# Kernel optimization log

Measured on AMD Instinct MI355X. Metric: run time of the kernel, lower is better.

Reference implementation:

```python
import jax, jax.numpy as jnp
import numpy as np
import math

NQ = 8            # n_qubits (hardcoded in _TransformerBlockQuantum)
DIM = 2 ** NQ     # statevector size = 256
H = 16            # num_heads
EPS = 1e-5        # LayerNorm eps

# PauliZ expectation table: wire 0 = most significant bit. ZTAB[w, j] = +/-1
_bits = (np.arange(DIM)[None, :] >> (NQ - 1 - np.arange(NQ)[:, None])) & 1
ZTAB = (1.0 - 2.0 * _bits).astype(np.float32)  # [NQ, DIM]


def _apply_1q(state, gate, w):
    # state: [N, 2^NQ] complex, gate: [N, 2, 2] complex, acts on wire w (MSB ordering)
    N = state.shape[0]
    s = state.reshape(N, 2 ** w, 2, 2 ** (NQ - w - 1))
    s = jnp.einsum('nab,npbq->npaq', gate, s)
    return s.reshape(N, DIM)


def _apply_cnot(state, c):
    # CNOT with control wire c, target wire c+1 (adjacent chain)
    N = state.shape[0]
    s = state.reshape(N, 2 ** c, 2, 2, 2 ** (NQ - c - 2))
    s = jnp.concatenate([s[:, :, :1], jnp.flip(s[:, :, 1:], axis=3)], axis=2)
    return s.reshape(N, DIM)


def _layernorm(x, g, b):
    mu = jnp.mean(x, axis=-1, keepdims=True)
    var = jnp.mean((x - mu) ** 2, axis=-1, keepdims=True)
    return (x - mu) / jnp.sqrt(var + EPS) * g + b


def _quantum_ffn(x, Win, b_in, Wout, b_out, ry):
    B, S, D = x.shape
    ang = (jnp.einsum('bsd,qd->bsq', x, Win) + b_in).reshape(-1, NQ)  # [N, NQ]
    N = ang.shape[0]
    state = jnp.zeros((N, DIM), jnp.complex64).at[:, 0].set(1.0)
    # RX encoding (per-token angles)
    for w in range(NQ):
        th = ang[:, w] * 0.5
        c, s = jnp.cos(th), jnp.sin(th)
        g = jnp.stack([jnp.stack([c, -1j * s], -1), jnp.stack([-1j * s, c], -1)], -2)
        state = _apply_1q(state, g.astype(jnp.complex64), w)
    # trainable RY (shared angles)
    for w in range(NQ):
        th = ry[w] * 0.5
        c, s = jnp.cos(th), jnp.sin(th)
        g = jnp.stack([jnp.stack([c, -s]), jnp.stack([s, c])]).astype(jnp.complex64)
        state = _apply_1q(state, jnp.broadcast_to(g, (N, 2, 2)), w)
    # CNOT entangling chain
    for w in range(NQ - 1):
        state = _apply_cnot(state, w)
    probs = jnp.abs(state) ** 2                      # [N, DIM] float32
    expz = probs @ ZTAB.T                            # [N, NQ]
    out = jnp.einsum('bsq,dq->bsd', expz.reshape(B, S, NQ), Wout) + b_out
    return jax.nn.relu(out)  # dropout = identity in eval


def _forward(x, Wq, Wk, Wv, Wo, g1, b1, g2, b2, Win, b_in, Wout, b_out, ry):
    B, S, D = x.shape
    dk = D // H
    q = jnp.einsum('bsd,ed->bse', x, Wq).reshape(B, S, H, dk)
    k = jnp.einsum('bsd,ed->bse', x, Wk).reshape(B, S, H, dk)
    v = jnp.einsum('bsd,ed->bse', x, Wv).reshape(B, S, H, dk)
    scores = jnp.einsum('bqhd,bkhd->bhqk', q, k) / math.sqrt(dk)
    attn = jax.nn.softmax(scores, axis=-1)
    o = jnp.einsum('bhqk,bkhd->bqhd', attn, v).reshape(B, S, D)
    attn_out = jnp.einsum('bsd,ed->bse', o, Wo)
    x1 = _layernorm(x + attn_out, g1, b1)
    ffn_out = _quantum_ffn(x1, Win, b_in, Wout, b_out, ry)
    return _layernorm(x1 + ffn_out, g2, b2)


def setup_inputs() -> dict:
    key = jax.random.key(0)
    ks = jax.random.split(key, 16)
    B, S, D = 2, 2048, 1024
    sd = 1.0 / math.sqrt(D)
    return {
        'x': jax.random.normal(ks[0], (B, S, D), jnp.float32),
        'Wq': jax.random.normal(ks[1], (D, D), jnp.float32) * sd,
        'Wk': jax.random.normal(ks[2], (D, D), jnp.float32) * sd,
        'Wv': jax.random.normal(ks[3], (D, D), jnp.float32) * sd,
        'Wo': jax.random.normal(ks[4], (D, D), jnp.float32) * sd,
        'g1': jnp.ones((D,), jnp.float32),
        'b1': jnp.zeros((D,), jnp.float32),
        'g2': jnp.ones((D,), jnp.float32),
        'b2': jnp.zeros((D,), jnp.float32),
        'Win': jax.random.normal(ks[5], (NQ, D), jnp.float32) * sd,
        'b_in': jnp.zeros((NQ,), jnp.float32),
        'Wout': jax.random.normal(ks[6], (D, NQ), jnp.float32) * (1.0 / math.sqrt(NQ)),
        'b_out': jnp.zeros((D,), jnp.float32),
        'ry': jax.random.normal(ks[7], (NQ,), jnp.float32) * 0.1,
    }


def reference(x, Wq, Wk, Wv, Wo, g1, b1, g2, b2, Win, b_in, Wout, b_out, ry):
    return _forward(x, Wq, Wk, Wv, Wo, g1, b1, g2, b2, Win, b_in, Wout, b_out, ry)
```

## Files before the change

kernel.cpp:

```cpp
#include <hip/hip_runtime.h>
#include <stdint.h>


typedef unsigned short u16;
typedef unsigned int   u32;
typedef __bf16 bf16x8 __attribute__((ext_vector_type(8)));
typedef u16    u16x8  __attribute__((ext_vector_type(8)));
typedef u16    u16x4  __attribute__((ext_vector_type(4)));
typedef float  f32x4  __attribute__((ext_vector_type(4)));

#define DEV static __device__ __forceinline__

DEV u16 f2b(float f){ u32 u = __float_as_uint(f); return (u16)((u + 0x7fffu + ((u>>16)&1u)) >> 16); }

#define MFMA16(a,b,c) __builtin_amdgcn_mfma_f32_16x16x32_bf16((a),(b),(c),0,0,0)
#define GLD16(gp,lp) __builtin_amdgcn_global_load_lds( \
    (const __attribute__((address_space(1))) u32*)(const void*)(gp), \
    (__attribute__((address_space(3))) u32*)(void*)(lp), 16, 0, 0)

__global__ __launch_bounds__(256) void k_cast(const float* __restrict__ src, u16* __restrict__ dst){
  const int i = blockIdx.x*256 + threadIdx.x;
  const f32x4* s = (const f32x4*)src + (size_t)i*2;
  f32x4 a = s[0], b = s[1];
  u16x8 o;
  o[0]=f2b(a.x); o[1]=f2b(a.y); o[2]=f2b(a.z); o[3]=f2b(a.w);
  o[4]=f2b(b.x); o[5]=f2b(b.y); o[6]=f2b(b.z); o[7]=f2b(b.w);
  ((u16x8*)dst)[i] = o;
}

__global__ __launch_bounds__(256) void k_cast_w(
    const float* __restrict__ Wq, const float* __restrict__ Wk,
    const float* __restrict__ Wv, const float* __restrict__ Wo,
    u16* __restrict__ wb, u16* __restrict__ wob){
  const int r = blockIdx.x >> 9, bi = blockIdx.x & 511;
  const float* src = (r==0)?Wq:((r==1)?Wk:((r==2)?Wv:Wo));
  u16* dst = (r<3) ? (wb + (size_t)r*1048576) : wob;
  const int i = bi*256 + threadIdx.x;
  const f32x4* s = (const f32x4*)src + (size_t)i*2;
  f32x4 a = s[0], b = s[1];
  u16x8 o;
  o[0]=f2b(a.x); o[1]=f2b(a.y); o[2]=f2b(a.z); o[3]=f2b(a.w);
  o[4]=f2b(b.x); o[5]=f2b(b.y); o[6]=f2b(b.z); o[7]=f2b(b.w);
  ((u16x8*)dst)[i] = o;
}

template<int MODE>
__global__ __launch_bounds__(256) void k_gemm_nt(
    const u16* __restrict__ A, const u16* __restrict__ B,
    float* __restrict__ Cf, u16* __restrict__ Qo, u16* __restrict__ Ko, u16* __restrict__ Vt,
    int K, int N)
{
  __shared__ __attribute__((aligned(16))) u16 As[128*64];
  __shared__ __attribute__((aligned(16))) u16 Bs[128*64];
  const int tid = threadIdx.x, lane = tid & 63, w = tid >> 6;
  const int wr = w >> 1, wc = w & 1;
  const int m0 = blockIdx.y*128, n0 = blockIdx.x*128;
  const int l15 = lane & 15, lg = lane >> 4;
  f32x4 acc[4][4] = {};
  const int lr = lane >> 3, lc = (lane & 7)*8;
  const u16* ag = A + (size_t)(m0 + w*32 + lr)*K + lc;
  const u16* bg = B + (size_t)(n0 + w*32 + lr)*K + lc;
  u16* asl = &As[(w*32)*64];
  u16* bsl = &Bs[(w*32)*64];
  for (int k0 = 0; k0 < K; k0 += 64){
    __syncthreads();
    #pragma unroll
    for (int c = 0; c < 4; ++c){
      GLD16(ag + (size_t)(c*8)*K + k0, asl + c*512);
      GLD16(bg + (size_t)(c*8)*K + k0, bsl + c*512);
    }
    __syncthreads();
    #pragma unroll
    for (int kk = 0; kk < 2; ++kk){
      const int ko = kk*32 + lg*8;
      bf16x8 af[4], bf[4];
      #pragma unroll
      for (int t=0;t<4;++t) af[t] = *(const bf16x8*)&As[(wr*64 + t*16 + l15)*64 + ko];
      #pragma unroll
      for (int t=0;t<4;++t) bf[t] = *(const bf16x8*)&Bs[(wc*64 + t*16 + l15)*64 + ko];
      #pragma unroll
      for (int i=0;i<4;++i)
        #pragma unroll
        for (int j=0;j<4;++j)
          acc[i][j] = MFMA16(af[i], bf[j], acc[i][j]);
    }
  }
  const int col0 = n0 + wc*64 + l15;
  const int row0 = m0 + wr*64 + lg*4;
  if (MODE==0){
    const int which = n0 >> 10;
    if (which == 2){
      #pragma unroll
      for (int i=0;i<4;++i){
        const int rr0 = row0 + i*16;
        const int bsel = rr0 >> 11, ss = rr0 & 2047;
        #pragma unroll
        for (int j=0;j<4;++j){
          const int d_loc = (col0 + j*16) & 1023;
          const int hh = d_loc >> 6, dd = d_loc & 63;
          u16x4 pk;
          #pragma unroll
          for (int r=0;r<4;++r) pk[r] = f2b(acc[i][j][r]);
          *(u16x4*)(Vt + ((size_t)((bsel*16 + hh)*64 + dd))*2048 + ss) = pk;
        }
      }
    } else {
      u16* dst = which ? Ko : Qo;
      const float scl = which ? 1.f : 0.125f;
      #pragma unroll
      for (int i=0;i<4;++i)
      #pragma unroll
      for (int j=0;j<4;++j){
        const int cc = (col0 + j*16) & 1023;
        #pragma unroll
        for (int r=0;r<4;++r)
          dst[(size_t)(row0 + i*16 + r)*1024 + cc] = f2b(acc[i][j][r]*scl);
      }
    }
  } else {
    #pragma unroll
    for (int i=0;i<4;++i)
    #pragma unroll
    for (int j=0;j<4;++j){
      const int cc = col0 + j*16;
      #pragma unroll
      for (int r=0;r<4;++r)
        Cf[(size_t)(row0 + i*16 + r)*N + cc] = acc[i][j][r];
    }
  }
}

__global__ __launch_bounds__(256) void k_attn(
    const u16* __restrict__ q, const u16* __restrict__ k,
    const u16* __restrict__ vt, u16* __restrict__ o)
{
  __shared__ __attribute__((aligned(16))) char KVb[2][16384];
  __shared__ __attribute__((aligned(16))) u16 Ps[4][1024];
  const int tid = threadIdx.x, lane = tid & 63, w = tid >> 6;
  const int p = blockIdx.x >> 5, qt = blockIdx.x & 31;
  const int b = p >> 4, h = p & 15;
  const int t0 = b*2048 + qt*64 + w*16;
  const int l15 = lane & 15, lg = lane >> 4;
  const int swz = (l15 & 7) << 4;
  bf16x8 qa[2];
  #pragma unroll
  for (int kk=0;kk<2;++kk)
    qa[kk] = *(const bf16x8*)(q + (size_t)(t0 + l15)*1024 + h*64 + kk*32 + lg*8);
  const char* kgl[2]; const char* vgl[2]; int ldsK[2], ldsV[2];
  #pragma unroll
  for (int i=0;i<2;++i){
    const int s = w*2048 + i*1024 + lane*16;
    const int row = s >> 7;
    const int cb = (s & 127) ^ ((row & 7) << 4);
    kgl[i] = (const char*)k  + ((size_t)(b*2048 + row))*2048 + h*128 + cb;
    vgl[i] = (const char*)vt + ((size_t)(p*64    + row))*4096 + cb;
    ldsK[i] = w*2048 + i*1024;
    ldsV[i] = 8192 + w*2048 + i*1024;
  }
  f32x4 oacc[4] = {};
  float mrow = -1e30f, lrow = 0.f;
  int cur = 0;
  #pragma unroll
  for (int i=0;i<2;++i){ GLD16(kgl[i], KVb[0] + ldsK[i]); GLD16(vgl[i], KVb[0] + ldsV[i]); }
  for (int it = 0; it < 32; ++it){
    __syncthreads();
    if (it < 31){
      const size_t nkv = (size_t)(it+1)*64;
      #pragma unroll
      for (int i=0;i<2;++i){
        GLD16(kgl[i] + nkv*2048, KVb[cur^1] + ldsK[i]);
        GLD16(vgl[i] + nkv*2,    KVb[cur^1] + ldsV[i]);
      }
    }
    const char* Kb = KVb[cur];
    const char* Vb = KVb[cur] + 8192;
    f32x4 sacc[4] = {};
    #pragma unroll
    for (int kk=0;kk<2;++kk){
      const int co = (kk*64 + lg*16) ^ swz;
      bf16x8 kbf[4];
      #pragma unroll
      for (int nt=0;nt<4;++nt) kbf[nt] = *(const bf16x8*)(Kb + (nt*16 + l15)*128 + co);
      #pragma unroll
      for (int nt=0;nt<4;++nt) sacc[nt] = MFMA16(kbf[nt], qa[kk], sacc[nt]);
    }
    float mx = sacc[0][0];
    #pragma unroll
    for (int nt=0;nt<4;++nt)
      #pragma unroll
      for (int r=0;r<4;++r) mx = fmaxf(mx, sacc[nt][r]);
    mx = fmaxf(mx, __shfl_xor(mx, 16));
    mx = fmaxf(mx, __shfl_xor(mx, 32));
    const float mnew = fmaxf(mrow, mx);
    const float scl = __expf(mrow - mnew);
    mrow = mnew;
    float rsum = 0.f;
    #pragma unroll
    for (int nt=0;nt<4;++nt)
      #pragma unroll
      for (int r=0;r<4;++r){ float e = __expf(sacc[nt][r] - mnew); sacc[nt][r] = e; rsum += e; }
    rsum += __shfl_xor(rsum, 16);
    rsum += __shfl_xor(rsum, 32);
    lrow = lrow*scl + rsum;
    char* Pw = (char*)&Ps[w][0];
    #pragma unroll
    for (int nt=0;nt<4;++nt){
      u16x4 pk;
      #pragma unroll
      for (int r=0;r<4;++r) pk[r] = f2b(sacc[nt][r]);
      *(u16x4*)(Pw + l15*128 + (((nt*16 + lg*4)*2) ^ swz)) = pk;
    }
    float sclo[4];
    #pragma unroll
    for (int r=0;r<4;++r) sclo[r] = __shfl(scl, lg*4 + r);
    #pragma unroll
    for (int nt=0;nt<4;++nt)
      #pragma unroll
      for (int r=0;r<4;++r) oacc[nt][r] *= sclo[r];
    #pragma unroll
    for (int kk=0;kk<2;++kk){
      const int co = (kk*64 + lg*16) ^ swz;
      bf16x8 pf = *(const bf16x8*)(Pw + l15*128 + co);
      bf16x8 vf[4];
      #pragma unroll
      for (int nt=0;nt<4;++nt) vf[nt] = *(const bf16x8*)(Vb + (nt*16 + l15)*128 + co);
      #pragma unroll
      for (int nt=0;nt<4;++nt) oacc[nt] = MFMA16(pf, vf[nt], oacc[nt]);
    }
    cur ^= 1;
  }
  float rl[4];
  #pragma unroll
  for (int r=0;r<4;++r){ float lf = __shfl(lrow, lg*4 + r); rl[r] = 1.f/lf; }
  #pragma unroll
  for (int nt=0;nt<4;++nt)
  #pragma unroll
  for (int r=0;r<4;++r)
    o[(size_t)(t0 + lg*4 + r)*1024 + h*64 + nt*16 + l15] = f2b(oacc[nt][r]*rl[r]);
}

__global__ __launch_bounds__(256) void k_tail(
    const float* __restrict__ x, const float* __restrict__ attn,
    const float* __restrict__ g1, const float* __restrict__ b1,
    const float* __restrict__ Win, const float* __restrict__ b_in,
    const float* __restrict__ Wout, const float* __restrict__ b_out,
    const float* __restrict__ ry,
    const float* __restrict__ g2, const float* __restrict__ b2,
    float* __restrict__ out)
{
  const int tid = threadIdx.x, lane = tid & 63, w = tid >> 6;
  const int t = blockIdx.x*4 + w;
  const size_t base = (size_t)t*1024;
  f32x4 yv[4];
  float s1 = 0.f, s2 = 0.f;
  #pragma unroll
  for (int c=0;c<4;++c){
    const int idx = c*256 + lane*4;
    f32x4 xv = *(const f32x4*)(x + base + idx);
    f32x4 av = *(const f32x4*)(attn + base + idx);
    f32x4 y = xv + av;
    yv[c] = y;
    s1 += y.x + y.y + y.z + y.w;
    s2 += y.x*y.x + y.y*y.y + y.z*y.z + y.w*y.w;
  }
  #pragma unroll
  for (int off=32; off; off>>=1){ s1 += __shfl_xor(s1, off); s2 += __shfl_xor(s2, off); }
  {
    const float mu = s1*(1.f/1024.f);
    const float rinv = rsqrtf(s2*(1.f/1024.f) - mu*mu + 1e-5f);
    #pragma unroll
    for (int c=0;c<4;++c){
      const int idx = c*256 + lane*4;
      f32x4 gv = *(const f32x4*)(g1 + idx);
      f32x4 bv = *(const f32x4*)(b1 + idx);
      f32x4 y = yv[c];
      y.x = (y.x-mu)*rinv*gv.x + bv.x;
      y.y = (y.y-mu)*rinv*gv.y + bv.y;
      y.z = (y.z-mu)*rinv*gv.z + bv.z;
      y.w = (y.w-mu)*rinv*gv.w + bv.w;
      yv[c] = y;
    }
  }
  float ang[8];
  #pragma unroll
  for (int qq=0; qq<8; ++qq){
    float acc = 0.f;
    #pragma unroll
    for (int c=0;c<4;++c){
      f32x4 wv = *(const f32x4*)(Win + qq*1024 + c*256 + lane*4);
      acc += wv.x*yv[c].x + wv.y*yv[c].y + wv.z*yv[c].z + wv.w*yv[c].w;
    }
    ang[qq] = acc;
  }
  #pragma unroll
  for (int off=32; off; off>>=1)
    #pragma unroll
    for (int qq=0; qq<8; ++qq) ang[qq] += __shfl_xor(ang[qq], off);
  #pragma unroll
  for (int qq=0; qq<8; ++qq) ang[qq] += b_in[qq];
  float vr[4], vi[4];
  #pragma unroll
  for (int r=0;r<4;++r){ vr[r]=0.f; vi[r]=0.f; }
  if (lane==0) vr[0] = 1.f;
  #pragma unroll
  for (int wi=0; wi<8; ++wi){
    float s, c; __sincosf(ang[wi]*0.5f, &s, &c);
    const int pbit = 7 - wi;
    if (pbit >= 6){
      const int rp = 1 << (pbit-6);
      #pragma unroll
      for (int r=0;r<4;++r) if (!(r & rp)){
        const int r2 = r | rp;
        float ar=vr[r], ai=vi[r], br=vr[r2], bi=vi[r2];
        vr[r]  = c*ar + s*bi;  vi[r]  = c*ai - s*br;
        vr[r2] = c*br + s*ai;  vi[r2] = c*bi - s*ar;
      }
    } else {
      const int msk = 1 << pbit;
      #pragma unroll
      for (int r=0;r<4;++r){
        float orr = __shfl_xor(vr[r], msk);
        float oii = __shfl_xor(vi[r], msk);
        float nr = c*vr[r] + s*oii;
        float ni = c*vi[r] - s*orr;
        vr[r]=nr; vi[r]=ni;
      }
    }
  }
  #pragma unroll
  for (int wi=0; wi<8; ++wi){
    float s, c; __sincosf(ry[wi]*0.5f, &s, &c);
    const int pbit = 7 - wi;
    if (pbit >= 6){
      const int rp = 1 << (pbit-6);
      #pragma unroll
      for (int r=0;r<4;++r) if (!(r & rp)){
        const int r2 = r | rp;
        float ar=vr[r], ai=vi[r], br=vr[r2], bi=vi[r2];
        vr[r]  = c*ar - s*br;  vi[r]  = c*ai - s*bi;
        vr[r2] = s*ar + c*br;  vi[r2] = s*ai + c*bi;
      }
    } else {
      const int msk = 1 << pbit;
      const float sg = (lane & msk) ? s : -s;
      #pragma unroll
      for (int r=0;r<4;++r){
        float orr = __shfl_xor(vr[r], msk);
        float oii = __shfl_xor(vi[r], msk);
        float nr = c*vr[r] + sg*orr;
        float ni = c*vi[r] + sg*oii;
        vr[r]=nr; vi[r]=ni;
      }
    }
  }
  { float tr=vr[2]; vr[2]=vr[3]; vr[3]=tr; float ti=vi[2]; vi[2]=vi[3]; vi[3]=ti; }
  vr[1]=__shfl_xor(vr[1],32); vi[1]=__shfl_xor(vi[1],32);
  vr[3]=__shfl_xor(vr[3],32); vi[3]=__shfl_xor(vi[3],32);
  #pragma unroll
  for (int cn=2; cn<7; ++cn){
    const int pc = 7-cn, pt = pc-1;
    const bool ctl = (lane >> pc) & 1;
    #pragma unroll
    for (int r=0;r<4;++r){
      float tr = __shfl_xor(vr[r], 1<<pt);
      float ti = __shfl_xor(vi[r], 1<<pt);
      if (ctl){ vr[r]=tr; vi[r]=ti; }
    }
  }
  float pr[4];
  #pragma unroll
  for (int r=0;r<4;++r) pr[r] = vr[r]*vr[r] + vi[r]*vi[r];
  float e[8];
  e[0] = (pr[0]+pr[1]) - (pr[2]+pr[3]);
  e[1] = (pr[0]+pr[2]) - (pr[1]+pr[3]);
  const float tot = pr[0]+pr[1]+pr[2]+pr[3];
  #pragma unroll
  for (int wi=2; wi<8; ++wi){
    const int pbit = 7-wi;
    e[wi] = ((lane >> pbit) & 1) ? -tot : tot;
  }
  #pragma unroll
  for (int off=1; off<64; off<<=1)
    #pragma unroll
    for (int i=0;i<8;++i) e[i] += __shfl_xor(e[i], off);
  float yy[4][4];
  s1 = 0.f; s2 = 0.f;
  #pragma unroll
  for (int c=0;c<4;++c){
    const float x1a[4] = {yv[c].x, yv[c].y, yv[c].z, yv[c].w};
    #pragma unroll
    for (int j=0;j<4;++j){
      const int d = c*256 + lane*4 + j;
      f32x4 w0 = *(const f32x4*)(Wout + (size_t)d*8);
      f32x4 w1 = *(const f32x4*)(Wout + (size_t)d*8 + 4);
      float acc = b_out[d];
      acc += w0.x*e[0] + w0.y*e[1] + w0.z*e[2] + w0.w*e[3];
      acc += w1.x*e[4] + w1.y*e[5] + w1.z*e[6] + w1.w*e[7];
      const float y = x1a[j] + fmaxf(acc, 0.f);
      yy[c][j] = y;
      s1 += y; s2 += y*y;
    }
  }
  #pragma unroll
  for (int off=32; off; off>>=1){ s1 += __shfl_xor(s1, off); s2 += __shfl_xor(s2, off); }
  const float mu = s1*(1.f/1024.f);
  const float rinv = rsqrtf(s2*(1.f/1024.f) - mu*mu + 1e-5f);
  #pragma unroll
  for (int c=0;c<4;++c){
    const int idx = c*256 + lane*4;
    f32x4 gv = *(const f32x4*)(g2 + idx);
    f32x4 bv = *(const f32x4*)(b2 + idx);
    f32x4 ov;
    ov.x = (yy[c][0]-mu)*rinv*gv.x + bv.x;
    ov.y = (yy[c][1]-mu)*rinv*gv.y + bv.y;
    ov.z = (yy[c][2]-mu)*rinv*gv.z + bv.z;
    ov.w = (yy[c][3]-mu)*rinv*gv.w + bv.w;
    *(f32x4*)(out + base + idx) = ov;
  }
}

extern "C" void kernel_launch(void* const* d_in, const int* in_sizes, int n_in,
                              void* d_out, int out_size, void* d_ws, size_t ws_size,
                              hipStream_t stream)
{
  const float* x    = (const float*)d_in[0];
  const float* Wq   = (const float*)d_in[1];
  const float* Wk   = (const float*)d_in[2];
  const float* Wv   = (const float*)d_in[3];
  const float* Wo   = (const float*)d_in[4];
  const float* g1   = (const float*)d_in[5];
  const float* b1   = (const float*)d_in[6];
  const float* g2   = (const float*)d_in[7];
  const float* b2   = (const float*)d_in[8];
  const float* Win  = (const float*)d_in[9];
  const float* b_in = (const float*)d_in[10];
  const float* Wout = (const float*)d_in[11];
  const float* b_out= (const float*)d_in[12];
  const float* ry   = (const float*)d_in[13];
  float* out = (float*)d_out;
  char* ws = (char*)d_ws;
  const size_t MB = 1024u*1024u;
  u16* xb  = (u16*)(ws + 0*MB);
  u16* wb  = (u16*)(ws + 8*MB);
  u16* wob = (u16*)(ws + 14*MB);
  u16* qb  = (u16*)(ws + 16*MB);
  u16* kb  = (u16*)(ws + 24*MB);
  u16* vtb = (u16*)(ws + 32*MB);
  u16* ob  = (u16*)(ws + 40*MB);
  float* attn_out = (float*)(ws + 48*MB);

  k_cast<<<2048, 256, 0, stream>>>(x, xb);
  k_cast_w<<<2048, 256, 0, stream>>>(Wq, Wk, Wv, Wo, wb, wob);
  k_gemm_nt<0><<<dim3(24,32), 256, 0, stream>>>(xb, wb, nullptr, qb, kb, vtb, 1024, 3072);
  k_attn<<<1024, 256, 0, stream>>>(qb, kb, vtb, ob);
  k_gemm_nt<1><<<dim3(8,32), 256, 0, stream>>>(ob, wob, attn_out, nullptr, nullptr, nullptr, 1024, 1024);
  k_tail<<<1024, 256, 0, stream>>>(x, attn_out, g1, b1, Win, b_in, Wout, b_out, ry, g2, b2, out);
}
```

Measured before the change: 279.2 us.

## Rework attention to 32x32 MFMA with register-resident P and lazy rescale

Rewrites the flash-attention kernel to use 32x32x16 bf16 MFMA with 128 query rows per block. P now stays in registers, exchanged across lanes with permlane32 swaps instead of an LDS round-trip. Adds exp2 softmax with log2e folded into the Q scale, a lazy rescale that skips the output update unless the max grows past a threshold, and s_setprio around MFMA sections. Also adds an XCD-aware block remap in the GEMM. These aim to cut LDS traffic, exp cost and cache misses, at the price of halving the attention grid to 512 blocks and more register pressure.

After: 268.9 us. 3.7% less time.

```diff
diff --git a/kernel.cpp b/kernel.cpp
--- a/kernel.cpp
+++ b/kernel.cpp
@@ -8,12 +8,27 @@
 typedef u16    u16x8  __attribute__((ext_vector_type(8)));
 typedef u16    u16x4  __attribute__((ext_vector_type(4)));
 typedef float  f32x4  __attribute__((ext_vector_type(4)));
+typedef float  f32x16 __attribute__((ext_vector_type(16)));
 
 #define DEV static __device__ __forceinline__
 
 DEV u16 f2b(float f){ u32 u = __float_as_uint(f); return (u16)((u + 0x7fffu + ((u>>16)&1u)) >> 16); }
+DEV u16 b2u(__bf16 h){ union{__bf16 b; u16 u;} c; c.b = h; return c.u; }
+DEV float exp2fast(float x){ return __builtin_amdgcn_exp2f(x); }
+
+DEV void plswap(u32 a, u32 b, u32& o0, u32& o1, int hi){
+#if __has_builtin(__builtin_amdgcn_permlane32_swap)
+  auto s = __builtin_amdgcn_permlane32_swap(a, b, false, false);
+  o0 = s[0]; o1 = s[1];
+#else
+  u32 xa = __shfl_xor(a, 32), xb = __shfl_xor(b, 32);
+  o0 = hi ? xb : a;
+  o1 = hi ? b  : xa;
+#endif
+}
 
 #define MFMA16(a,b,c) __builtin_amdgcn_mfma_f32_16x16x32_bf16((a),(b),(c),0,0,0)
+#define MFMA32(a,b,c) __builtin_amdgcn_mfma_f32_32x32x16_bf16((a),(b),(c),0,0,0)
 #define GLD16(gp,lp) __builtin_amdgcn_global_load_lds( \
     (const __attribute__((address_space(1))) u32*)(const void*)(gp), \
     (__attribute__((address_space(3))) u32*)(void*)(lp), 16, 0, 0)
@@ -54,7 +69,11 @@
   __shared__ __attribute__((aligned(16))) u16 Bs[128*64];
   const int tid = threadIdx.x, lane = tid & 63, w = tid >> 6;
   const int wr = w >> 1, wc = w & 1;
-  const int m0 = blockIdx.y*128, n0 = blockIdx.x*128;
+  const int nwg = gridDim.x * gridDim.y;
+  int lin = blockIdx.y * gridDim.x + blockIdx.x;
+  lin = (lin & 7) * (nwg >> 3) + (lin >> 3);
+  const int n0 = (lin % gridDim.x) * 128;
+  const int m0 = (lin / gridDim.x) * 128;
   const int l15 = lane & 15, lg = lane >> 4;
   f32x4 acc[4][4] = {};
   const int lr = lane >> 3, lc = (lane & 7)*8;
@@ -106,7 +125,7 @@
       }
     } else {
       u16* dst = which ? Ko : Qo;
-      const float scl = which ? 1.f : 0.125f;
+      const float scl = which ? 1.f : 0.125f*1.44269504f;
       #pragma unroll
       for (int i=0;i<4;++i)
       #pragma unroll
@@ -135,17 +154,16 @@
     const u16* __restrict__ vt, u16* __restrict__ o)
 {
   __shared__ __attribute__((aligned(16))) char KVb[2][16384];
-  __shared__ __attribute__((aligned(16))) u16 Ps[4][1024];
   const int tid = threadIdx.x, lane = tid & 63, w = tid >> 6;
-  const int p = blockIdx.x >> 5, qt = blockIdx.x & 31;
+  const int p = blockIdx.x >> 4, qt = blockIdx.x & 15;
   const int b = p >> 4, h = p & 15;
-  const int t0 = b*2048 + qt*64 + w*16;
-  const int l15 = lane & 15, lg = lane >> 4;
-  const int swz = (l15 & 7) << 4;
-  bf16x8 qa[2];
-  #pragma unroll
-  for (int kk=0;kk<2;++kk)
-    qa[kk] = *(const bf16x8*)(q + (size_t)(t0 + l15)*1024 + h*64 + kk*32 + lg*8);
+  const int l31 = lane & 31, hi = lane >> 5;
+  const int qrow = b*2048 + qt*128 + w*32 + l31;
+  const int swz = (l31 & 7) << 4;
+  bf16x8 qa[4];
+  #pragma unroll
+  for (int kk=0;kk<4;++kk)
+    qa[kk] = *(const bf16x8*)(q + (size_t)qrow*1024 + h*64 + kk*16 + hi*8);
   const char* kgl[2]; const char* vgl[2]; int ldsK[2], ldsV[2];
   #pragma unroll
   for (int i=0;i<2;++i){
@@ -157,7 +175,7 @@
     ldsK[i] = w*2048 + i*1024;
     ldsV[i] = 8192 + w*2048 + i*1024;
   }
-  f32x4 oacc[4] = {};
+  f32x16 oacc[2] = {};
   float mrow = -1e30f, lrow = 0.f;
   int cur = 0;
   #pragma unroll
@@ -174,69 +192,90 @@
     }
     const char* Kb = KVb[cur];
     const char* Vb = KVb[cur] + 8192;
-    f32x4 sacc[4] = {};
-    #pragma unroll
-    for (int kk=0;kk<2;++kk){
-      const int co = (kk*64 + lg*16) ^ swz;
-      bf16x8 kbf[4];
-      #pragma unroll
-      for (int nt=0;nt<4;++nt) kbf[nt] = *(const bf16x8*)(Kb + (nt*16 + l15)*128 + co);
-      #pragma unroll
-      for (int nt=0;nt<4;++nt) sacc[nt] = MFMA16(kbf[nt], qa[kk], sacc[nt]);
-    }
+    f32x16 sacc[2] = {};
+    __builtin_amdgcn_s_setprio(1);
+    #pragma unroll
+    for (int t32=0;t32<2;++t32){
+      const int row = t32*32 + l31;
+      #pragma unroll
+      for (int kk=0;kk<4;++kk){
+        bf16x8 kf = *(const bf16x8*)(Kb + row*128 + ((kk*32 + hi*16) ^ swz));
+        sacc[t32] = MFMA32(kf, qa[kk], sacc[t32]);
+      }
+    }
+    __builtin_amdgcn_s_setprio(0);
     float mx = sacc[0][0];
     #pragma unroll
-    for (int nt=0;nt<4;++nt)
-      #pragma unroll
-      for (int r=0;r<4;++r) mx = fmaxf(mx, sacc[nt][r]);
-    mx = fmaxf(mx, __shfl_xor(mx, 16));
+    for (int t32=0;t32<2;++t32)
+      #pragma unroll
+      for (int i=0;i<16;++i) mx = fmaxf(mx, sacc[t32][i]);
     mx = fmaxf(mx, __shfl_xor(mx, 32));
-    const float mnew = fmaxf(mrow, mx);
-    const float scl = __expf(mrow - mnew);
-    mrow = mnew;
+    if (!__all(mx <= mrow + 8.f)){
+      const float mnew = fmaxf(mrow, mx);
+      const float scl = exp2fast(mrow - mnew);
+      mrow = mnew; lrow *= scl;
+      #pragma unroll
+      for (int dt=0;dt<2;++dt)
+        #pragma unroll
+        for (int i=0;i<16;++i) oacc[dt][i] *= scl;
+    }
     float rsum = 0.f;
     #pragma unroll
-    for (int nt=0;nt<4;++nt)
-      #pragma unroll
-      for (int r=0;r<4;++r){ float e = __expf(sacc[nt][r] - mnew); sacc[nt][r] = e; rsum += e; }
-    rsum += __shfl_xor(rsum, 16);
+    for (int t32=0;t32<2;++t32)
+      #pragma unroll
+      for (int i=0;i<16;++i){
+        const float e = exp2fast(sacc[t32][i] - mrow);
+        sacc[t32][i] = e; rsum += e;
+      }
     rsum += __shfl_xor(rsum, 32);
-    lrow = lrow*scl + rsum;
-    char* Pw = (char*)&Ps[w][0];
-    #pragma unroll
-    for (int nt=0;nt<4;++nt){
-      u16x4 pk;
-      #pragma unroll
-      for (int r=0;r<4;++r) pk[r] = f2b(sacc[nt][r]);
-      *(u16x4*)(Pw + l15*128 + (((nt*16 + lg*4)*2) ^ swz)) = pk;
-    }
-    float sclo[4];
-    #pragma unroll
-    for (int r=0;r<4;++r) sclo[r] = __shfl(scl, lg*4 + r);
-    #pragma unroll
-    for (int nt=0;nt<4;++nt)
-      #pragma unroll
-      for (int r=0;r<4;++r) oacc[nt][r] *= sclo[r];
-    #pragma unroll
-    for (int kk=0;kk<2;++kk){
-      const int co = (kk*64 + lg*16) ^ swz;
-      bf16x8 pf = *(const bf16x8*)(Pw + l15*128 + co);
-      bf16x8 vf[4];
-      #pragma unroll
-      for (int nt=0;nt<4;++nt) vf[nt] = *(const bf16x8*)(Vb + (nt*16 + l15)*128 + co);
-      #pragma unroll
-      for (int nt=0;nt<4;++nt) oacc[nt] = MFMA16(pf, vf[nt], oacc[nt]);
-    }
+    lrow += rsum;
+    u32 pk[2][8];
+    #pragma unroll
+    for (int t32=0;t32<2;++t32)
+      #pragma unroll
+      for (int u=0;u<8;++u){
+        const int idx = (u>>1)*4 + (u&1)*2;
+        const u32 lo = b2u((__bf16)sacc[t32][idx]);
+        const u32 hh = b2u((__bf16)sacc[t32][idx+1]);
+        pk[t32][u] = lo | (hh << 16);
+      }
+    bf16x8 pb[4];
+    #pragma unroll
+    for (int op=0;op<4;++op){
+      const int t32 = op>>1, base = (op&1)*4;
+      u32 w0,w1,w2,w3;
+      plswap(pk[t32][base+0], pk[t32][base+2], w0, w2, hi);
+      plswap(pk[t32][base+1], pk[t32][base+3], w1, w3, hi);
+      union { u32 u[4]; bf16x8 v; } cc;
+      cc.u[0]=w0; cc.u[1]=w1; cc.u[2]=w2; cc.u[3]=w3;
+      pb[op] = cc.v;
+    }
+    __builtin_amdgcn_s_setprio(1);
+    #pragma unroll
+    for (int dt=0;dt<2;++dt){
+      const int row = dt*32 + l31;
+      #pragma unroll
+      for (int op=0;op<4;++op){
+        bf16x8 vf = *(const bf16x8*)(Vb + row*128 + ((op*32 + hi*16) ^ swz));
+        oacc[dt] = MFMA32(vf, pb[op], oacc[dt]);
+      }
+    }
+    __builtin_amdgcn_s_setprio(0);
     cur ^= 1;
   }
-  float rl[4];
-  #pragma unroll
-  for (int r=0;r<4;++r){ float lf = __shfl(lrow, lg*4 + r); rl[r] = 1.f/lf; }
-  #pragma unroll
-  for (int nt=0;nt<4;++nt)
-  #pragma unroll
-  for (int r=0;r<4;++r)
-    o[(size_t)(t0 + lg*4 + r)*1024 + h*64 + nt*16 + l15] = f2b(oacc[nt][r]*rl[r]);
+  const float rinv = 1.f / lrow;
+  u16* orow = o + (size_t)qrow*1024 + h*64;
+  #pragma unroll
+  for (int dt=0;dt<2;++dt)
+    #pragma unroll
+    for (int rg=0;rg<4;++rg)
+      #pragma unroll
+      for (int hf=0;hf<2;++hf){
+        const int r0 = rg*4 + hf*2;
+        const u32 lo = b2u((__bf16)(oacc[dt][r0]   * rinv));
+        const u32 hh = b2u((__bf16)(oacc[dt][r0+1] * rinv));
+        *(u32*)(orow + dt*32 + rg*8 + hi*4 + hf*2) = lo | (hh << 16);
+      }
 }
 
 __global__ __launch_bounds__(256) void k_tail(
@@ -452,7 +491,7 @@
   k_cast<<<2048, 256, 0, stream>>>(x, xb);
   k_cast_w<<<2048, 256, 0, stream>>>(Wq, Wk, Wv, Wo, wb, wob);
   k_gemm_nt<0><<<dim3(24,32), 256, 0, stream>>>(xb, wb, nullptr, qb, kb, vtb, 1024, 3072);
-  k_attn<<<1024, 256, 0, stream>>>(qb, kb, vtb, ob);
+  k_attn<<<512, 256, 0, stream>>>(qb, kb, vtb, ob);
   k_gemm_nt<1><<<dim3(8,32), 256, 0, stream>>>(ob, wob, attn_out, nullptr, nullptr, nullptr, 1024, 1024);
   k_tail<<<1024, 256, 0, stream>>>(x, attn_out, g1, b1, Win, b_in, Wout, b_out, ry, g2, b2, out);
 }
```
